# Kernel optimization log

Measured on AMD Instinct MI355X. Metric: run time of the kernel, lower is better.

Reference implementation:

```python
import jax, jax.numpy as jnp
import numpy as np

B, T, J, D = 128, 256, 50, 3
I, H, C = J * D, 1024, 60


def setup_inputs() -> dict:
    key = jax.random.key(0)
    ks = jax.random.split(key, 10)
    s = 0.02
    return {
        "x": jax.random.normal(ks[0], (B, T, J, D), dtype=jnp.float32),
        "h1": jnp.zeros((B, H), jnp.float32),
        "c1": jnp.zeros((B, H), jnp.float32),
        "h2": jnp.zeros((B, H), jnp.float32),
        "c2": jnp.zeros((B, H), jnp.float32),
        "W_ih1": jax.random.normal(ks[1], (4 * H, I), jnp.float32) * s,
        "W_hh1": jax.random.normal(ks[2], (4 * H, H), jnp.float32) * s,
        "b_ih1": jax.random.normal(ks[3], (4 * H,), jnp.float32) * s,
        "b_hh1": jax.random.normal(ks[4], (4 * H,), jnp.float32) * s,
        "W_ih2": jax.random.normal(ks[5], (4 * H, H), jnp.float32) * s,
        "W_hh2": jax.random.normal(ks[6], (4 * H, H), jnp.float32) * s,
        "b_ih2": jax.random.normal(ks[7], (4 * H,), jnp.float32) * s,
        "b_hh2": jax.random.normal(ks[8], (4 * H,), jnp.float32) * s,
        "W_fc": jax.random.normal(ks[9], (C, H), jnp.float32) * s,
        "b_fc": jnp.zeros((C,), jnp.float32),
        "mode": 0,  # 0 == 'val' (no dropout), static
    }


def _lstm_cell(xv, h, c, Wih, Whh, bih, bhh):
    # PyTorch LSTMCell gate order: i, f, g, o
    gates = xv @ Wih.T + bih + h @ Whh.T + bhh  # [B, 4H]
    i, f, g, o = jnp.split(gates, 4, axis=-1)
    c_new = jax.nn.sigmoid(f) * c + jax.nn.sigmoid(i) * jnp.tanh(g)
    h_new = jax.nn.sigmoid(o) * jnp.tanh(c_new)
    return h_new, c_new


def reference(x, h1, c1, h2, c2, W_ih1, W_hh1, b_ih1, b_hh1,
              W_ih2, W_hh2, b_ih2, b_hh2, W_fc, b_fc, mode):
    b, t = x.shape[0], x.shape[1]
    xs = x.reshape(b, t, -1).transpose(1, 0, 2)  # [T, B, I]

    def step(carry, xt):
        h1, c1, h2, c2 = carry
        h1, c1 = _lstm_cell(xt, h1, c1, W_ih1, W_hh1, b_ih1, b_hh1)
        # mode==0 ('val'): no dropout between layers
        h2, c2 = _lstm_cell(h1, h2, c2, W_ih2, W_hh2, b_ih2, b_hh2)
        return (h1, c1, h2, c2), None

    (h1, c1, h2, c2), _ = jax.lax.scan(step, (h1, c1, h2, c2), xs)
    return h2 @ W_fc.T + b_fc  # [B, num_class]
```

## Files before the change

### kernel.cpp

```cpp
#include <hip/hip_runtime.h>
#include <math.h>


typedef __bf16 bf16;
typedef __bf16 bf16x8 __attribute__((ext_vector_type(8)));
typedef float floatx4 __attribute__((ext_vector_type(4)));
typedef unsigned long long ull;

#define B_   128
#define T_   256
#define H_   1024
#define I_   150
#define KX_  160
#define C_   60
#define K1LDS 1280
#define KP    1024
#define NLINES 40
#define CSTRIDE 64
#define FLAGLINE 16
#define L0FLAG 32
#define L1FLAG 33
#define NCOLS 32
#define NHC  8
#define NT   2

template<int N> struct IC { static constexpr int value = N; };

__device__ __forceinline__ float sigmoidf_(float x) { return 1.f / (1.f + expf(-x)); }

__global__ __launch_bounds__(256)
void convert_all(const float* __restrict__ x,
                 const float* __restrict__ h1in, const float* __restrict__ h2in,
                 bf16* __restrict__ xb, bf16* __restrict__ h1b0, bf16* __restrict__ h2b0,
                 unsigned* __restrict__ cnt)
{
    const size_t nXB = (size_t)T_ * B_ * KX_;
    const size_t nHC = (size_t)B_ * H_;
    size_t idx = (size_t)blockIdx.x * 256 + threadIdx.x;

    if (idx < nXB) {
        size_t t = idx / (B_ * KX_);
        size_t r = idx - t * (B_ * KX_);
        size_t b = r / KX_, k = r - b * KX_;
        xb[idx] = (k < I_) ? (bf16)x[(b * T_ + t) * I_ + k] : (bf16)0.f;
        return;
    }
    idx -= nXB;
    if (idx < nHC) { h1b0[idx] = (bf16)h1in[idx]; return; }
    idx -= nHC;
    if (idx < nHC) { h2b0[idx] = (bf16)h2in[idx]; return; }
    idx -= nHC;
    if (idx < NLINES * CSTRIDE) cnt[idx] = 0u;
}

__device__ __forceinline__ void stage_rebal(
    bf16* lds, bf16* ldsP, int tid, int layer, int n0h,
    const float* Wih1, const float* Whh1, const float* Wih2, const float* Whh2)
{
    if (layer == 0) {
        {
            const int cpr = K1LDS >> 3;
            const int total = NCOLS * cpr;
            for (int ci = tid; ci < total; ci += 512) {
                int r = ci / cpr, c = ci - r * cpr;
                int g = r / NHC, j = r - g * NHC;
                int grow = (g << 10) + n0h + j;
                int k0 = c << 3;
                float v[8];
#pragma unroll
                for (int u = 0; u < 8; ++u) {
                    int k = k0 + u;
                    v[u] = (k < I_) ? Wih1[(size_t)grow * I_ + k]
                         : (k < KX_) ? 0.f
                         : (k < KX_ + H_) ? Whh1[(size_t)grow * H_ + (k - KX_)] : 0.f;
                }
                int cs = (c & ~15) | ((c ^ r) & 15);
                bf16* dst = lds + (size_t)r * K1LDS + (cs << 3);
#pragma unroll
                for (int u = 0; u < 8; ++u) dst[u] = (bf16)v[u];
            }
        }
        {
            const int cpr = KP >> 3;
            const int total = NCOLS * cpr;
            for (int ci = tid; ci < total; ci += 512) {
                int r = ci / cpr, c = ci - r * cpr;
                int g = r / NHC, j = r - g * NHC;
                int grow = (g << 10) + n0h + j;
                int k0 = c << 3;
                float v[8];
#pragma unroll
                for (int u = 0; u < 8; ++u) v[u] = Wih2[(size_t)grow * H_ + k0 + u];
                int cs = (c & ~15) | ((c ^ r) & 15);
                bf16* dst = ldsP + (size_t)r * KP + (cs << 3);
#pragma unroll
                for (int u = 0; u < 8; ++u) dst[u] = (bf16)v[u];
            }
        }
    } else {
        const int cpr = KP >> 3;
        const int total = NCOLS * cpr;
        for (int ci = tid; ci < total; ci += 512) {
            int r = ci / cpr, c = ci - r * cpr;
            int g = r / NHC, j = r - g * NHC;
            int grow = (g << 10) + n0h + j;
            int k0 = c << 3;
            float v[8];
#pragma unroll
            for (int u = 0; u < 8; ++u) v[u] = Whh2[(size_t)grow * H_ + k0 + u];
            int cs = (c & ~15) | ((c ^ r) & 15);
            bf16* dst = lds + (size_t)r * KP + (cs << 3);
#pragma unroll
            for (int u = 0; u < 8; ++u) dst[u] = (bf16)v[u];
        }
    }
}

__global__ __launch_bounds__(512, 2)
void rnn_decoup8(const bf16* __restrict__ xb,
                 bf16* __restrict__ h1b0, bf16* __restrict__ h1b1,
                 bf16* __restrict__ h2b0, bf16* __restrict__ h2b1,
                 float* __restrict__ p0, float* __restrict__ p1, float* __restrict__ p2,
                 const float* __restrict__ c1in, const float* __restrict__ c2in,
                 const float* __restrict__ Wih1, const float* __restrict__ Whh1,
                 const float* __restrict__ bih1, const float* __restrict__ bhh1,
                 const float* __restrict__ Wih2, const float* __restrict__ Whh2,
                 const float* __restrict__ bih2, const float* __restrict__ bhh2,
                 const float* __restrict__ Wfc, const float* __restrict__ bfc,
                 float* __restrict__ out, unsigned* __restrict__ cnt, int nblk)
{
    extern __shared__ bf16 lds[];
    __shared__ __align__(16) bf16 hst[8][16][NHC];

    const int tid   = threadIdx.x;
    const int bid   = blockIdx.x;
    const int layer = (bid >> 3) & 1;
    const int slice = (bid & 7) | ((bid >> 4) << 3);
    const int n0h   = slice * NHC;
    const int line  = layer * 16 + ((bid & 7) | (((bid >> 4) & 1) << 3));
    bf16* ldsP = lds + 32 * K1LDS;

    stage_rebal(lds, ldsP, tid, layer, n0h, Wih1, Whh1, Wih2, Whh2);
    __syncthreads();

    const int lane = tid & 63;
    const int wv   = tid >> 6;
    const int jj   = lane & (NHC - 1);
    const int quad = lane >> 4;

    float4 bias;
    {
        const float* bi = layer ? bih2 : bih1;
        const float* bh = layer ? bhh2 : bhh1;
        int col = n0h + jj;
        bias.x = bi[col] + bh[col];
        bias.y = bi[col + H_] + bh[col + H_];
        bias.z = bi[col + 2 * H_] + bh[col + 2 * H_];
        bias.w = bi[col + 3 * H_] + bh[col + 3 * H_];
    }

    float creg[2];
    {
        const float* cin = layer ? c2in : c1in;
        int dup = (lane >> 3) & 1;
#pragma unroll
        for (int rp = 0; rp < 2; ++rp) {
            int row = wv * 16 + quad * 4 + rp * 2 + dup;
            creg[rp] = cin[(size_t)row * H_ + n0h + jj];
        }
    }

    floatx4 acc[NT];
    floatx4 pacc[NT];

    auto seg1 = [&](const bf16* A, int ldA, const bf16* Bb, int ldB,
                    auto nksC, int ksBase) {
        constexpr int NKS = decltype(nksC)::value;
        constexpr int CH  = NKS < 16 ? NKS : 16;
        const int arow = wv * 16 + (lane & 15);
        const bf16* a0 = A + (size_t)arow * ldA + quad * 8;
        for (int blk = 0; blk < NKS; blk += CH) {
            bf16x8 a0r[CH];
#pragma unroll
            for (int i = 0; i < CH; ++i)
                a0r[i] = *(const bf16x8*)(a0 + (blk + i) * 32);
            __builtin_amdgcn_sched_barrier(0);
#pragma unroll
            for (int i = 0; i < CH; ++i) {
                int c = (ksBase + blk + i) * 4 + quad;
#pragma unroll
                for (int t = 0; t < NT; ++t) {
                    int r = t * 16 + (lane & 15);
                    int cs = (c & ~15) | ((c ^ r) & 15);
                    bf16x8 bfr = *(const bf16x8*)(Bb + (size_t)r * ldB + (cs << 3));
                    acc[t] = __builtin_amdgcn_mfma_f32_16x16x32_bf16(a0r[i], bfr, acc[t], 0, 0, 0);
                }
            }
        }
    };

    auto segDual = [&](const bf16* A) {
        const int arow = wv * 16 + (lane & 15);
        const bf16* a0 = A + (size_t)arow * H_ + quad * 8;
        for (int blk = 0; blk < 32; blk += 16) {
            bf16x8 a0r[16];
#pragma unroll
            for (int i = 0; i < 16; ++i)
                a0r[i] = *(const bf16x8*)(a0 + (blk + i) * 32);
            __builtin_amdgcn_sched_barrier(0);
#pragma unroll
            for (int i = 0; i < 16; ++i) {
                int ig = blk + i;
                int c1 = (5 + ig) * 4 + quad;
                int cp = ig * 4 + quad;
#pragma unroll
                for (int t = 0; t < NT; ++t) {
                    int r = t * 16 + (lane & 15);
                    int cs1 = (c1 & ~15) | ((c1 ^ r) & 15);
                    bf16x8 b1 = *(const bf16x8*)(lds + (size_t)r * K1LDS + (cs1 << 3));
                    acc[t] = __builtin_amdgcn_mfma_f32_16x16x32_bf16(a0r[i], b1, acc[t], 0, 0, 0);
                    int csp = (cp & ~15) | ((cp ^ r) & 15);
                    bf16x8 bp = *(const bf16x8*)(ldsP + (size_t)r * KP + (csp << 3));
                    pacc[t] = __builtin_amdgcn_mfma_f32_16x16x32_bf16(a0r[i], bp, pacc[t], 0, 0, 0);
                }
            }
        }
    };

    auto epilogue = [&](bf16* hw) {
        const int base = lane & 48;
#pragma unroll
        for (int r = 0; r < 4; ++r) {
            float vi = __shfl(acc[0][r], base + jj, 64);
            float vf = __shfl(acc[0][r], base + 8 + jj, 64);
            float vg = __shfl(acc[1][r], base + jj, 64);
            float vo = __shfl(acc[1][r], base + 8 + jj, 64);
            bool cond = (((lane >> 3) & 1) == (r & 1));
            int slot = r >> 1;
            if (cond) {
                float cv = creg[slot];
                float cn = sigmoidf_(vf + bias.y) * cv
                         + sigmoidf_(vi + bias.x) * tanhf(vg + bias.z);
                creg[slot] = cn;
                float hn = sigmoidf_(vo + bias.w) * tanhf(cn);
                hst[wv][quad * 4 + r][jj] = (bf16)hn;
            }
        }
        __syncthreads();
        if (lane < 32) {
            int row_l = lane >> 1, cg = lane & 1;
            ull v = *(const ull*)&hst[wv][row_l][cg * 4];
            __hip_atomic_store((ull*)(hw + (size_t)(wv * 16 + row_l) * H_ + n0h + cg * 4),
                               v, __ATOMIC_RELAXED, __HIP_MEMORY_SCOPE_AGENT);
        }
    };

    if (layer == 0) {
#pragma unroll
        for (int t = 0; t < NT; ++t) {
            acc[t]  = (floatx4){0.f, 0.f, 0.f, 0.f};
            pacc[t] = (floatx4){0.f, 0.f, 0.f, 0.f};
        }
        seg1(xb, KX_, lds, K1LDS, IC<5>{}, 0);
    }

    for (int e = 0; e <= T_ + 1; ++e) {
        const int pm  = e % 3;
        const int pmr = (e + 2) % 3;
        float* const pbuf[3] = { p0, p1, p2 };

        if (layer == 0 && e <= T_) {
            const bf16* h1r = (e & 1) ? h1b1 : h1b0;
            segDual(h1r);

            float* pw = pbuf[pm] + (size_t)slice * B_ * NCOLS;
#pragma unroll
            for (int t = 0; t < NT; ++t)
#pragma unroll
                for (int r = 0; r < 4; ++r) {
                    int row = wv * 16 + quad * 4 + r;
                    __hip_atomic_store(pw + (size_t)row * NCOLS + t * 16 + (lane & 15),
                                       pacc[t][r], __ATOMIC_RELAXED, __HIP_MEMORY_SCOPE_AGENT);
                }

            if (e < T_) {
                bf16* hw = (e & 1) ? h1b0 : h1b1;
                epilogue(hw);
            }
        } else if (layer == 1 && e >= 2) {
#pragma unroll
            for (int t = 0; t < NT; ++t) acc[t] = (floatx4){0.f, 0.f, 0.f, 0.f};

            const float* pr = pbuf[pmr] + (size_t)slice * B_ * NCOLS;
            float pv[NT][4];
#pragma unroll
            for (int t = 0; t < NT; ++t)
#pragma unroll
                for (int r = 0; r < 4; ++r) {
                    int row = wv * 16 + quad * 4 + r;
                    pv[t][r] = pr[(size_t)row * NCOLS + t * 16 + (lane & 15)];
                }

            const bf16* h2r = (e & 1) ? h2b1 : h2b0;
            seg1(h2r, H_, lds, KP, IC<32>{}, 0);

#pragma unroll
            for (int t = 0; t < NT; ++t)
#pragma unroll
                for (int r = 0; r < 4; ++r) acc[t][r] += pv[t][r];

            bf16* hw = (e & 1) ? h2b0 : h2b1;
            epilogue(hw);
        }

        asm volatile("s_waitcnt vmcnt(0)" ::: "memory");
        __syncthreads();
        const int etag = e + 1;
        if (tid == 0)
            __hip_atomic_fetch_add(cnt + line * CSTRIDE, 1u,
                                   __ATOMIC_RELAXED, __HIP_MEMORY_SCOPE_AGENT);
        if (layer == 0 && e < T_) {
#pragma unroll
            for (int t = 0; t < NT; ++t) {
                acc[t]  = (floatx4){0.f, 0.f, 0.f, 0.f};
                pacc[t] = (floatx4){0.f, 0.f, 0.f, 0.f};
            }
            if (e + 1 < T_)
                seg1(xb + (size_t)(e + 1) * B_ * KX_, KX_, lds, K1LDS, IC<5>{}, 0);
        }
        if (layer == 0) {
            if (bid == 0) {
                if (tid < 16) {
                    const unsigned tgt = 8u * (unsigned)etag;
                    const unsigned* cp = cnt + tid * CSTRIDE;
                    while (__hip_atomic_load(cp, __ATOMIC_RELAXED, __HIP_MEMORY_SCOPE_AGENT) < tgt)
                        __builtin_amdgcn_s_sleep(1);
                }
                if (tid == 0)
                    __hip_atomic_store(cnt + L0FLAG * CSTRIDE, (unsigned)etag,
                                       __ATOMIC_RELAXED, __HIP_MEMORY_SCOPE_AGENT);
            } else if (tid == 0) {
                const unsigned* fp = cnt + L0FLAG * CSTRIDE;
                while (__hip_atomic_load(fp, __ATOMIC_RELAXED, __HIP_MEMORY_SCOPE_AGENT) < (unsigned)etag)
                    __builtin_amdgcn_s_sleep(1);
            }
            if (tid == 0 && etag >= 3) {
                const unsigned* fp = cnt + L1FLAG * CSTRIDE;
                while (__hip_atomic_load(fp, __ATOMIC_RELAXED, __HIP_MEMORY_SCOPE_AGENT) < (unsigned)(etag - 2))
                    __builtin_amdgcn_s_sleep(1);
            }
        } else {
            if (bid == 8) {
                if (tid < 16) {
                    const unsigned tgt = 8u * (unsigned)etag;
                    const unsigned* cp = cnt + (16 + tid) * CSTRIDE;
                    while (__hip_atomic_load(cp, __ATOMIC_RELAXED, __HIP_MEMORY_SCOPE_AGENT) < tgt)
                        __builtin_amdgcn_s_sleep(1);
                }
                if (tid == 0)
                    __hip_atomic_store(cnt + L1FLAG * CSTRIDE, (unsigned)etag,
                                       __ATOMIC_RELAXED, __HIP_MEMORY_SCOPE_AGENT);
            } else if (tid == 0) {
                const unsigned* fp = cnt + L1FLAG * CSTRIDE;
                while (__hip_atomic_load(fp, __ATOMIC_RELAXED, __HIP_MEMORY_SCOPE_AGENT) < (unsigned)etag)
                    __builtin_amdgcn_s_sleep(1);
            }
            if (tid == 0) {
                const unsigned* fp = cnt + L0FLAG * CSTRIDE;
                while (__hip_atomic_load(fp, __ATOMIC_RELAXED, __HIP_MEMORY_SCOPE_AGENT) < (unsigned)etag)
                    __builtin_amdgcn_s_sleep(1);
            }
        }
        __syncthreads();
        if (tid < 64)
            __builtin_amdgcn_fence(__ATOMIC_ACQUIRE, "agent");
        __syncthreads();
    }

    if (tid == 0 && layer == 0) {
        const unsigned* fp = cnt + L1FLAG * CSTRIDE;
        while (__hip_atomic_load(fp, __ATOMIC_RELAXED, __HIP_MEMORY_SCOPE_AGENT) < (unsigned)(T_ + 2))
            __builtin_amdgcn_s_sleep(1);
    }
    __syncthreads();
    if (tid < 64)
        __builtin_amdgcn_fence(__ATOMIC_ACQUIRE, "agent");
    __syncthreads();

    if (bid < B_) {
        const bf16* h2f = h2b0;
        for (int c = wv; c < C_; c += 8) {
            float a = 0.f;
            for (int k = lane; k < H_; k += 64)
                a += (float)h2f[(size_t)bid * H_ + k] * Wfc[(size_t)c * H_ + k];
#pragma unroll
            for (int off = 32; off; off >>= 1) a += __shfl_down(a, off, 64);
            if (lane == 0) out[bid * C_ + c] = a + bfc[c];
        }
    }
}

__global__ __launch_bounds__(512, 2)
void rnn_rebal8(const bf16* __restrict__ xb,
                bf16* __restrict__ h1b0, bf16* __restrict__ h1b1,
                bf16* __restrict__ h2b0, bf16* __restrict__ h2b1,
                float* __restrict__ p0, float* __restrict__ p1,
                const float* __restrict__ c1in, const float* __restrict__ c2in,
                const float* __restrict__ Wih1, const float* __restrict__ Whh1,
                const float* __restrict__ bih1, const float* __restrict__ bhh1,
                const float* __restrict__ Wih2, const float* __restrict__ Whh2,
                const float* __restrict__ bih2, const float* __restrict__ bhh2,
                const float* __restrict__ Wfc, const float* __restrict__ bfc,
                float* __restrict__ out, unsigned* __restrict__ cnt, int nblk)
{
    extern __shared__ bf16 lds[];
    __shared__ __align__(16) bf16 hst[8][16][NHC];

    const int tid   = threadIdx.x;
    const int bid   = blockIdx.x;
    const int layer = (bid >> 3) & 1;
    const int slice = (bid & 7) | ((bid >> 4) << 3);
    const int n0h   = slice * NHC;
    const int arr_per_line = nblk >> 4;
    bf16* ldsP = lds + 32 * K1LDS;

    stage_rebal(lds, ldsP, tid, layer, n0h, Wih1, Whh1, Wih2, Whh2);
    __syncthreads();

    const int lane = tid & 63;
    const int wv   = tid >> 6;
    const int jj   = lane & (NHC - 1);
    const int quad = lane >> 4;

    float4 bias;
    {
        const float* bi = layer ? bih2 : bih1;
        const float* bh = layer ? bhh2 : bhh1;
        int col = n0h + jj;
        bias.x = bi[col] + bh[col];
        bias.y = bi[col + H_] + bh[col + H_];
        bias.z = bi[col + 2 * H_] + bh[col + 2 * H_];
        bias.w = bi[col + 3 * H_] + bh[col + 3 * H_];
    }

    float creg[2];
    {
        const float* cin = layer ? c2in : c1in;
        int dup = (lane >> 3) & 1;
#pragma unroll
        for (int rp = 0; rp < 2; ++rp) {
            int row = wv * 16 + quad * 4 + rp * 2 + dup;
            creg[rp] = cin[(size_t)row * H_ + n0h + jj];
        }
    }

    floatx4 acc[NT];
    floatx4 pacc[NT];

    auto seg1 = [&](const bf16* A, int ldA, const bf16* Bb, int ldB,
                    auto nksC, int ksBase) {
        constexpr int NKS = decltype(nksC)::value;
        constexpr int CH  = NKS < 16 ? NKS : 16;
        const int arow = wv * 16 + (lane & 15);
        const bf16* a0 = A + (size_t)arow * ldA + quad * 8;
        for (int blk = 0; blk < NKS; blk += CH) {
            bf16x8 a0r[CH];
#pragma unroll
            for (int i = 0; i < CH; ++i)
                a0r[i] = *(const bf16x8*)(a0 + (blk + i) * 32);
            __builtin_amdgcn_sched_barrier(0);
#pragma unroll
            for (int i = 0; i < CH; ++i) {
                int c = (ksBase + blk + i) * 4 + quad;
#pragma unroll
                for (int t = 0; t < NT; ++t) {
                    int r = t * 16 + (lane & 15);
                    int cs = (c & ~15) | ((c ^ r) & 15);
                    bf16x8 bfr = *(const bf16x8*)(Bb + (size_t)r * ldB + (cs << 3));
                    acc[t] = __builtin_amdgcn_mfma_f32_16x16x32_bf16(a0r[i], bfr, acc[t], 0, 0, 0);
                }
            }
        }
    };

    auto segDual = [&](const bf16* A) {
        const int arow = wv * 16 + (lane & 15);
        const bf16* a0 = A + (size_t)arow * H_ + quad * 8;
        for (int blk = 0; blk < 32; blk += 16) {
            bf16x8 a0r[16];
#pragma unroll
            for (int i = 0; i < 16; ++i)
                a0r[i] = *(const bf16x8*)(a0 + (blk + i) * 32);
            __builtin_amdgcn_sched_barrier(0);
#pragma unroll
            for (int i = 0; i < 16; ++i) {
                int ig = blk + i;
                int c1 = (5 + ig) * 4 + quad;
                int cp = ig * 4 + quad;
#pragma unroll
                for (int t = 0; t < NT; ++t) {
                    int r = t * 16 + (lane & 15);
                    int cs1 = (c1 & ~15) | ((c1 ^ r) & 15);
                    bf16x8 b1 = *(const bf16x8*)(lds + (size_t)r * K1LDS + (cs1 << 3));
                    acc[t] = __builtin_amdgcn_mfma_f32_16x16x32_bf16(a0r[i], b1, acc[t], 0, 0, 0);
                    int csp = (cp & ~15) | ((cp ^ r) & 15);
                    bf16x8 bp = *(const bf16x8*)(ldsP + (size_t)r * KP + (csp << 3));
                    pacc[t] = __builtin_amdgcn_mfma_f32_16x16x32_bf16(a0r[i], bp, pacc[t], 0, 0, 0);
                }
            }
        }
    };

    auto epilogue = [&](bf16* hw) {
        const int base = lane & 48;
#pragma unroll
        for (int r = 0; r < 4; ++r) {
            float vi = __shfl(acc[0][r], base + jj, 64);
            float vf = __shfl(acc[0][r], base + 8 + jj, 64);
            float vg = __shfl(acc[1][r], base + jj, 64);
            float vo = __shfl(acc[1][r], base + 8 + jj, 64);
            bool cond = (((lane >> 3) & 1) == (r & 1));
            int slot = r >> 1;
            if (cond) {
                float cv = creg[slot];
                float cn = sigmoidf_(vf + bias.y) * cv
                         + sigmoidf_(vi + bias.x) * tanhf(vg + bias.z);
                creg[slot] = cn;
                float hn = sigmoidf_(vo + bias.w) * tanhf(cn);
                hst[wv][quad * 4 + r][jj] = (bf16)hn;
            }
        }
        __syncthreads();
        if (lane < 32) {
            int row_l = lane >> 1, cg = lane & 1;
            ull v = *(const ull*)&hst[wv][row_l][cg * 4];
            __hip_atomic_store((ull*)(hw + (size_t)(wv * 16 + row_l) * H_ + n0h + cg * 4),
                               v, __ATOMIC_RELAXED, __HIP_MEMORY_SCOPE_AGENT);
        }
    };

    if (layer == 0) {
#pragma unroll
        for (int t = 0; t < NT; ++t) {
            acc[t]  = (floatx4){0.f, 0.f, 0.f, 0.f};
            pacc[t] = (floatx4){0.f, 0.f, 0.f, 0.f};
        }
        seg1(xb, KX_, lds, K1LDS, IC<5>{}, 0);
    }

    for (int e = 0; e <= T_ + 1; ++e) {
        if (layer == 0 && e <= T_) {
            const bf16* h1r = (e & 1) ? h1b1 : h1b0;
            segDual(h1r);

            float* pw = ((e & 1) ? p1 : p0) + (size_t)slice * B_ * NCOLS;
#pragma unroll
            for (int t = 0; t < NT; ++t)
#pragma unroll
                for (int r = 0; r < 4; ++r) {
                    int row = wv * 16 + quad * 4 + r;
                    __hip_atomic_store(pw + (size_t)row * NCOLS + t * 16 + (lane & 15),
                                       pacc[t][r], __ATOMIC_RELAXED, __HIP_MEMORY_SCOPE_AGENT);
                }

            if (e < T_) {
                bf16* hw = (e & 1) ? h1b0 : h1b1;
                epilogue(hw);
            }
        } else if (layer == 1 && e >= 2) {
#pragma unroll
            for (int t = 0; t < NT; ++t) acc[t] = (floatx4){0.f, 0.f, 0.f, 0.f};

            const float* pr = ((e & 1) ? p0 : p1) + (size_t)slice * B_ * NCOLS;
            float pv[NT][4];
#pragma unroll
            for (int t = 0; t < NT; ++t)
#pragma unroll
                for (int r = 0; r < 4; ++r) {
                    int row = wv * 16 + quad * 4 + r;
                    pv[t][r] = pr[(size_t)row * NCOLS + t * 16 + (lane & 15)];
                }

            const bf16* h2r = (e & 1) ? h2b1 : h2b0;
            seg1(h2r, H_, lds, KP, IC<32>{}, 0);

#pragma unroll
            for (int t = 0; t < NT; ++t)
#pragma unroll
                for (int r = 0; r < 4; ++r) acc[t][r] += pv[t][r];

            bf16* hw = (e & 1) ? h2b0 : h2b1;
            epilogue(hw);
        }

        asm volatile("s_waitcnt vmcnt(0)" ::: "memory");
        __syncthreads();
        const unsigned etag = (unsigned)(e + 1);
        if (tid == 0)
            __hip_atomic_fetch_add(cnt + (bid & 15) * CSTRIDE, 1u,
                                   __ATOMIC_RELAXED, __HIP_MEMORY_SCOPE_AGENT);
        if (layer == 0 && e < T_) {
#pragma unroll
            for (int t = 0; t < NT; ++t) {
                acc[t]  = (floatx4){0.f, 0.f, 0.f, 0.f};
                pacc[t] = (floatx4){0.f, 0.f, 0.f, 0.f};
            }
            if (e + 1 < T_)
                seg1(xb + (size_t)(e + 1) * B_ * KX_, KX_, lds, K1LDS, IC<5>{}, 0);
        }
        if (bid == 0) {
            if (tid < 16) {
                const unsigned tgt = etag * (unsigned)arr_per_line;
                const unsigned* cp = cnt + tid * CSTRIDE;
                while (__hip_atomic_load(cp, __ATOMIC_RELAXED, __HIP_MEMORY_SCOPE_AGENT) < tgt)
                    __builtin_amdgcn_s_sleep(1);
            }
            if (tid == 0)
                __hip_atomic_store(cnt + FLAGLINE * CSTRIDE, etag,
                                   __ATOMIC_RELAXED, __HIP_MEMORY_SCOPE_AGENT);
        } else {
            if (tid == 0) {
                const unsigned* fp = cnt + FLAGLINE * CSTRIDE;
                while (__hip_atomic_load(fp, __ATOMIC_RELAXED, __HIP_MEMORY_SCOPE_AGENT) < etag)
                    __builtin_amdgcn_s_sleep(1);
            }
        }
        __syncthreads();
        if (tid < 64)
            __builtin_amdgcn_fence(__ATOMIC_ACQUIRE, "agent");
        __syncthreads();
    }

    if (bid < B_) {
        const bf16* h2f = h2b0;
        for (int c = wv; c < C_; c += 8) {
            float a = 0.f;
            for (int k = lane; k < H_; k += 64)
                a += (float)h2f[(size_t)bid * H_ + k] * Wfc[(size_t)c * H_ + k];
#pragma unroll
            for (int off = 32; off; off >>= 1) a += __shfl_down(a, off, 64);
            if (lane == 0) out[bid * C_ + c] = a + bfc[c];
        }
    }
}

extern "C" void kernel_launch(void* const* d_in, const int* in_sizes, int n_in,
                              void* d_out, int out_size, void* d_ws, size_t ws_size,
                              hipStream_t stream)
{
    const float* x    = (const float*)d_in[0];
    const float* h1in = (const float*)d_in[1];
    const float* c1in = (const float*)d_in[2];
    const float* h2in = (const float*)d_in[3];
    const float* c2in = (const float*)d_in[4];
    const float* Wih1 = (const float*)d_in[5];
    const float* Whh1 = (const float*)d_in[6];
    const float* bih1 = (const float*)d_in[7];
    const float* bhh1 = (const float*)d_in[8];
    const float* Wih2 = (const float*)d_in[9];
    const float* Whh2 = (const float*)d_in[10];
    const float* bih2 = (const float*)d_in[11];
    const float* bhh2 = (const float*)d_in[12];
    const float* Wfc  = (const float*)d_in[13];
    const float* bfc  = (const float*)d_in[14];
    float* out = (float*)d_out;

    const size_t szXB  = (size_t)T_ * B_ * KX_ * 2;
    const size_t szH   = (size_t)B_ * H_ * 2;
    const size_t szCnt = (size_t)NLINES * CSTRIDE * 4;
    const size_t szP   = (size_t)128 * B_ * NCOLS * 4;
    const size_t needR13 = szXB + 4 * szH + szCnt + 2 * szP;
    const size_t needDec = szXB + 4 * szH + szCnt + 3 * szP;

    char* p = (char*)d_ws;
    bf16* xb = (bf16*)p;    p += szXB;
    bf16* h1b0 = (bf16*)p;  p += szH;
    bf16* h1b1 = (bf16*)p;  p += szH;
    bf16* h2b0 = (bf16*)p;  p += szH;
    bf16* h2b1 = (bf16*)p;  p += szH;
    unsigned* cnt = (unsigned*)p;  p += szCnt;
    float* p0 = (float*)p;  p += szP;
    float* p1 = (float*)p;  p += szP;
    float* p2 = (float*)p;

    const size_t citems = (size_t)T_ * B_ * KX_ + 2 * (size_t)B_ * H_ + NLINES * CSTRIDE;
    convert_all<<<(int)((citems + 255) / 256), 256, 0, stream>>>(
        x, h1in, h2in, xb, h1b0, h2b0, cnt);

    int nblk = 256;
    void* argsDec[] = { &xb, &h1b0, &h1b1, &h2b0, &h2b1, &p0, &p1, &p2,
                        (void*)&c1in, (void*)&c2in,
                        (void*)&Wih1, (void*)&Whh1, (void*)&bih1, (void*)&bhh1,
                        (void*)&Wih2, (void*)&Whh2, (void*)&bih2, (void*)&bhh2,
                        (void*)&Wfc, (void*)&bfc, &out, &cnt, &nblk };
    void* argsR13[] = { &xb, &h1b0, &h1b1, &h2b0, &h2b1, &p0, &p1,
                        (void*)&c1in, (void*)&c2in,
                        (void*)&Wih1, (void*)&Whh1, (void*)&bih1, (void*)&bhh1,
                        (void*)&Wih2, (void*)&Whh2, (void*)&bih2, (void*)&bhh2,
                        (void*)&Wfc, (void*)&bfc, &out, &cnt, &nblk };

    const unsigned ldsRebal = (unsigned)(32 * K1LDS + 32 * KP) * 2u;
    hipError_t err = hipErrorOutOfMemory;
    if (ws_size >= needDec) {
        if (hipFuncSetAttribute((const void*)rnn_decoup8,
                                hipFuncAttributeMaxDynamicSharedMemorySize,
                                (int)ldsRebal) == hipSuccess) {
            err = hipLaunchCooperativeKernel((const void*)rnn_decoup8,
                                             dim3(256), dim3(512), argsDec,
                                             ldsRebal, stream);
        }
    }
    if (err != hipSuccess && ws_size >= needR13) {
        (void)hipGetLastError();
        if (hipFuncSetAttribute((const void*)rnn_rebal8,
                                hipFuncAttributeMaxDynamicSharedMemorySize,
                                (int)ldsRebal) == hipSuccess) {
            (void)hipLaunchCooperativeKernel((const void*)rnn_rebal8,
                                             dim3(256), dim3(512), argsR13,
                                             ldsRebal, stream);
        }
    }
}
```

Measured before the change: 3.330 ms.

## Replace leader-based grid barrier with distributed per-line counter polling

```diff
diff --git a/kernel.cpp b/kernel.cpp
--- a/kernel.cpp
+++ b/kernel.cpp
@@ -17,7 +17,6 @@
 #define KP    1024
 #define NLINES 40
 #define CSTRIDE 64
-#define FLAGLINE 16
 #define L0FLAG 32
 #define L1FLAG 33
 #define NCOLS 32
@@ -112,6 +111,271 @@
             bf16* dst = lds + (size_t)r * KP + (cs << 3);
 #pragma unroll
             for (int u = 0; u < 8; ++u) dst[u] = (bf16)v[u];
+        }
+    }
+}
+
+__global__ __launch_bounds__(512, 2)
+void rnn_dist8(const bf16* __restrict__ xb,
+               bf16* __restrict__ h1b0, bf16* __restrict__ h1b1,
+               bf16* __restrict__ h2b0, bf16* __restrict__ h2b1,
+               float* __restrict__ p0, float* __restrict__ p1, float* __restrict__ p2,
+               const float* __restrict__ c1in, const float* __restrict__ c2in,
+               const float* __restrict__ Wih1, const float* __restrict__ Whh1,
+               const float* __restrict__ bih1, const float* __restrict__ bhh1,
+               const float* __restrict__ Wih2, const float* __restrict__ Whh2,
+               const float* __restrict__ bih2, const float* __restrict__ bhh2,
+               const float* __restrict__ Wfc, const float* __restrict__ bfc,
+               float* __restrict__ out, unsigned* __restrict__ cnt, int nblk)
+{
+    extern __shared__ bf16 lds[];
+    __shared__ __align__(16) bf16 hst[8][16][NHC];
+
+    const int tid   = threadIdx.x;
+    const int bid   = blockIdx.x;
+    const int layer = (bid >> 3) & 1;
+    const int slice = (bid & 7) | ((bid >> 4) << 3);
+    const int n0h   = slice * NHC;
+    const int line  = layer * 16 + ((bid & 7) | (((bid >> 4) & 1) << 3));
+    bf16* ldsP = lds + 32 * K1LDS;
+
+    stage_rebal(lds, ldsP, tid, layer, n0h, Wih1, Whh1, Wih2, Whh2);
+    __syncthreads();
+
+    const int lane = tid & 63;
+    const int wv   = tid >> 6;
+    const int jj   = lane & (NHC - 1);
+    const int quad = lane >> 4;
+
+    float4 bias;
+    {
+        const float* bi = layer ? bih2 : bih1;
+        const float* bh = layer ? bhh2 : bhh1;
+        int col = n0h + jj;
+        bias.x = bi[col] + bh[col];
+        bias.y = bi[col + H_] + bh[col + H_];
+        bias.z = bi[col + 2 * H_] + bh[col + 2 * H_];
+        bias.w = bi[col + 3 * H_] + bh[col + 3 * H_];
+    }
+
+    float creg[2];
+    {
+        const float* cin = layer ? c2in : c1in;
+        int dup = (lane >> 3) & 1;
+#pragma unroll
+        for (int rp = 0; rp < 2; ++rp) {
+            int row = wv * 16 + quad * 4 + rp * 2 + dup;
+            creg[rp] = cin[(size_t)row * H_ + n0h + jj];
+        }
+    }
+
+    floatx4 acc[NT];
+    floatx4 pacc[NT];
+
+    auto seg1 = [&](const bf16* A, int ldA, const bf16* Bb, int ldB,
+                    auto nksC, int ksBase) {
+        constexpr int NKS = decltype(nksC)::value;
+        constexpr int CH  = NKS < 16 ? NKS : 16;
+        const int arow = wv * 16 + (lane & 15);
+        const bf16* a0 = A + (size_t)arow * ldA + quad * 8;
+        for (int blk = 0; blk < NKS; blk += CH) {
+            bf16x8 a0r[CH];
+#pragma unroll
+            for (int i = 0; i < CH; ++i)
+                a0r[i] = *(const bf16x8*)(a0 + (blk + i) * 32);
+            __builtin_amdgcn_sched_barrier(0);
+#pragma unroll
+            for (int i = 0; i < CH; ++i) {
+                int c = (ksBase + blk + i) * 4 + quad;
+#pragma unroll
+                for (int t = 0; t < NT; ++t) {
+                    int r = t * 16 + (lane & 15);
+                    int cs = (c & ~15) | ((c ^ r) & 15);
+                    bf16x8 bfr = *(const bf16x8*)(Bb + (size_t)r * ldB + (cs << 3));
+                    acc[t] = __builtin_amdgcn_mfma_f32_16x16x32_bf16(a0r[i], bfr, acc[t], 0, 0, 0);
+                }
+            }
+        }
+    };
+
+    auto segDual = [&](const bf16* A) {
+        const int arow = wv * 16 + (lane & 15);
+        const bf16* a0 = A + (size_t)arow * H_ + quad * 8;
+        for (int blk = 0; blk < 32; blk += 16) {
+            bf16x8 a0r[16];
+#pragma unroll
+            for (int i = 0; i < 16; ++i)
+                a0r[i] = *(const bf16x8*)(a0 + (blk + i) * 32);
+            __builtin_amdgcn_sched_barrier(0);
+#pragma unroll
+            for (int i = 0; i < 16; ++i) {
+                int ig = blk + i;
+                int c1 = (5 + ig) * 4 + quad;
+                int cp = ig * 4 + quad;
+#pragma unroll
+                for (int t = 0; t < NT; ++t) {
+                    int r = t * 16 + (lane & 15);
+                    int cs1 = (c1 & ~15) | ((c1 ^ r) & 15);
+                    bf16x8 b1 = *(const bf16x8*)(lds + (size_t)r * K1LDS + (cs1 << 3));
+                    acc[t] = __builtin_amdgcn_mfma_f32_16x16x32_bf16(a0r[i], b1, acc[t], 0, 0, 0);
+                    int csp = (cp & ~15) | ((cp ^ r) & 15);
+                    bf16x8 bp = *(const bf16x8*)(ldsP + (size_t)r * KP + (csp << 3));
+                    pacc[t] = __builtin_amdgcn_mfma_f32_16x16x32_bf16(a0r[i], bp, pacc[t], 0, 0, 0);
+                }
+            }
+        }
+    };
+
+    auto epilogue = [&](bf16* hw) {
+        const int base = lane & 48;
+#pragma unroll
+        for (int r = 0; r < 4; ++r) {
+            float vi = __shfl(acc[0][r], base + jj, 64);
+            float vf = __shfl(acc[0][r], base + 8 + jj, 64);
+            float vg = __shfl(acc[1][r], base + jj, 64);
+            float vo = __shfl(acc[1][r], base + 8 + jj, 64);
+            bool cond = (((lane >> 3) & 1) == (r & 1));
+            int slot = r >> 1;
+            if (cond) {
+                float cv = creg[slot];
+                float cn = sigmoidf_(vf + bias.y) * cv
+                         + sigmoidf_(vi + bias.x) * tanhf(vg + bias.z);
+                creg[slot] = cn;
+                float hn = sigmoidf_(vo + bias.w) * tanhf(cn);
+                hst[wv][quad * 4 + r][jj] = (bf16)hn;
+            }
+        }
+        __syncthreads();
+        if (lane < 32) {
+            int row_l = lane >> 1, cg = lane & 1;
+            ull v = *(const ull*)&hst[wv][row_l][cg * 4];
+            __hip_atomic_store((ull*)(hw + (size_t)(wv * 16 + row_l) * H_ + n0h + cg * 4),
+                               v, __ATOMIC_RELAXED, __HIP_MEMORY_SCOPE_AGENT);
+        }
+    };
+
+    if (layer == 0) {
+#pragma unroll
+        for (int t = 0; t < NT; ++t) {
+            acc[t]  = (floatx4){0.f, 0.f, 0.f, 0.f};
+            pacc[t] = (floatx4){0.f, 0.f, 0.f, 0.f};
+        }
+        seg1(xb, KX_, lds, K1LDS, IC<5>{}, 0);
+    }
+
+    for (int e = 0; e <= T_ + 1; ++e) {
+        const int pm  = e % 3;
+        const int pmr = (e + 2) % 3;
+        float* const pbuf[3] = { p0, p1, p2 };
+
+        if (layer == 0 && e <= T_) {
+            const bf16* h1r = (e & 1) ? h1b1 : h1b0;
+            segDual(h1r);
+
+            float* pw = pbuf[pm] + (size_t)slice * B_ * NCOLS;
+#pragma unroll
+            for (int t = 0; t < NT; ++t)
+#pragma unroll
+                for (int r = 0; r < 4; ++r) {
+                    int row = wv * 16 + quad * 4 + r;
+                    __hip_atomic_store(pw + (size_t)row * NCOLS + t * 16 + (lane & 15),
+                                       pacc[t][r], __ATOMIC_RELAXED, __HIP_MEMORY_SCOPE_AGENT);
+                }
+
+            if (e < T_) {
+                bf16* hw = (e & 1) ? h1b0 : h1b1;
+                epilogue(hw);
+            }
+        } else if (layer == 1 && e >= 2) {
+#pragma unroll
+            for (int t = 0; t < NT; ++t) acc[t] = (floatx4){0.f, 0.f, 0.f, 0.f};
+
+            const float* pr = pbuf[pmr] + (size_t)slice * B_ * NCOLS;
+            float pv[NT][4];
+#pragma unroll
+            for (int t = 0; t < NT; ++t)
+#pragma unroll
+                for (int r = 0; r < 4; ++r) {
+                    int row = wv * 16 + quad * 4 + r;
+                    pv[t][r] = pr[(size_t)row * NCOLS + t * 16 + (lane & 15)];
+                }
+
+            const bf16* h2r = (e & 1) ? h2b1 : h2b0;
+            seg1(h2r, H_, lds, KP, IC<32>{}, 0);
+
+#pragma unroll
+            for (int t = 0; t < NT; ++t)
+#pragma unroll
+                for (int r = 0; r < 4; ++r) acc[t][r] += pv[t][r];
+
+            bf16* hw = (e & 1) ? h2b0 : h2b1;
+            epilogue(hw);
+        }
+
+        asm volatile("s_waitcnt vmcnt(0)" ::: "memory");
+        __syncthreads();
+        const int etag = e + 1;
+        if (tid == 0)
+            __hip_atomic_fetch_add(cnt + line * CSTRIDE, 1u,
+                                   __ATOMIC_RELAXED, __HIP_MEMORY_SCOPE_AGENT);
+        if (layer == 0 && e < T_) {
+#pragma unroll
+            for (int t = 0; t < NT; ++t) {
+                acc[t]  = (floatx4){0.f, 0.f, 0.f, 0.f};
+                pacc[t] = (floatx4){0.f, 0.f, 0.f, 0.f};
+            }
+            if (e + 1 < T_)
+                seg1(xb + (size_t)(e + 1) * B_ * KX_, KX_, lds, K1LDS, IC<5>{}, 0);
+        }
+        if (tid < 64) {
+            const unsigned* cp = nullptr;
+            unsigned tgt = 0;
+            if (lane < 16) {
+                cp = cnt + (layer * 16 + lane) * CSTRIDE;
+                tgt = 8u * (unsigned)etag;
+            } else if (lane < 32) {
+                if (layer == 0) {
+                    if (etag >= 3) {
+                        cp = cnt + (16 + (lane - 16)) * CSTRIDE;
+                        tgt = 8u * (unsigned)(etag - 2);
+                    }
+                } else {
+                    cp = cnt + (lane - 16) * CSTRIDE;
+                    tgt = 8u * (unsigned)etag;
+                }
+            }
+            for (;;) {
+                bool ok = (cp == nullptr) ||
+                          (__hip_atomic_load(cp, __ATOMIC_RELAXED,
+                                             __HIP_MEMORY_SCOPE_AGENT) >= tgt);
+                if (__all(ok)) break;
+                __builtin_amdgcn_s_sleep(1);
+            }
+            __builtin_amdgcn_fence(__ATOMIC_ACQUIRE, "agent");
+        }
+        __syncthreads();
+    }
+
+    if (tid < 64) {
+        if (lane < 16) {
+            const unsigned* cp = cnt + (16 + lane) * CSTRIDE;
+            while (__hip_atomic_load(cp, __ATOMIC_RELAXED,
+                                     __HIP_MEMORY_SCOPE_AGENT) < 8u * (unsigned)(T_ + 2))
+                __builtin_amdgcn_s_sleep(1);
+        }
+        __builtin_amdgcn_fence(__ATOMIC_ACQUIRE, "agent");
+    }
+    __syncthreads();
+
+    if (bid < B_) {
+        const bf16* h2f = h2b0;
+        for (int c = wv; c < C_; c += 8) {
+            float a = 0.f;
+            for (int k = lane; k < H_; k += 64)
+                a += (float)h2f[(size_t)bid * H_ + k] * Wfc[(size_t)c * H_ + k];
+#pragma unroll
+            for (int off = 32; off; off >>= 1) a += __shfl_down(a, off, 64);
+            if (lane == 0) out[bid * C_ + c] = a + bfc[c];
         }
     }
 }
@@ -386,250 +650,6 @@
     if (tid < 64)
         __builtin_amdgcn_fence(__ATOMIC_ACQUIRE, "agent");
     __syncthreads();
-
-    if (bid < B_) {
-        const bf16* h2f = h2b0;
-        for (int c = wv; c < C_; c += 8) {
-            float a = 0.f;
-            for (int k = lane; k < H_; k += 64)
-                a += (float)h2f[(size_t)bid * H_ + k] * Wfc[(size_t)c * H_ + k];
-#pragma unroll
-            for (int off = 32; off; off >>= 1) a += __shfl_down(a, off, 64);
-            if (lane == 0) out[bid * C_ + c] = a + bfc[c];
-        }
-    }
-}
-
-__global__ __launch_bounds__(512, 2)
-void rnn_rebal8(const bf16* __restrict__ xb,
-                bf16* __restrict__ h1b0, bf16* __restrict__ h1b1,
-                bf16* __restrict__ h2b0, bf16* __restrict__ h2b1,
-                float* __restrict__ p0, float* __restrict__ p1,
-                const float* __restrict__ c1in, const float* __restrict__ c2in,
-                const float* __restrict__ Wih1, const float* __restrict__ Whh1,
-                const float* __restrict__ bih1, const float* __restrict__ bhh1,
-                const float* __restrict__ Wih2, const float* __restrict__ Whh2,
-                const float* __restrict__ bih2, const float* __restrict__ bhh2,
-                const float* __restrict__ Wfc, const float* __restrict__ bfc,
-                float* __restrict__ out, unsigned* __restrict__ cnt, int nblk)
-{
-    extern __shared__ bf16 lds[];
-    __shared__ __align__(16) bf16 hst[8][16][NHC];
-
-    const int tid   = threadIdx.x;
-    const int bid   = blockIdx.x;
-    const int layer = (bid >> 3) & 1;
-    const int slice = (bid & 7) | ((bid >> 4) << 3);
-    const int n0h   = slice * NHC;
-    const int arr_per_line = nblk >> 4;
-    bf16* ldsP = lds + 32 * K1LDS;
-
-    stage_rebal(lds, ldsP, tid, layer, n0h, Wih1, Whh1, Wih2, Whh2);
-    __syncthreads();
-
-    const int lane = tid & 63;
-    const int wv   = tid >> 6;
-    const int jj   = lane & (NHC - 1);
-    const int quad = lane >> 4;
-
-    float4 bias;
-    {
-        const float* bi = layer ? bih2 : bih1;
-        const float* bh = layer ? bhh2 : bhh1;
-        int col = n0h + jj;
-        bias.x = bi[col] + bh[col];
-        bias.y = bi[col + H_] + bh[col + H_];
-        bias.z = bi[col + 2 * H_] + bh[col + 2 * H_];
-        bias.w = bi[col + 3 * H_] + bh[col + 3 * H_];
-    }
-
-    float creg[2];
-    {
-        const float* cin = layer ? c2in : c1in;
-        int dup = (lane >> 3) & 1;
-#pragma unroll
-        for (int rp = 0; rp < 2; ++rp) {
-            int row = wv * 16 + quad * 4 + rp * 2 + dup;
-            creg[rp] = cin[(size_t)row * H_ + n0h + jj];
-        }
-    }
-
-    floatx4 acc[NT];
-    floatx4 pacc[NT];
-
-    auto seg1 = [&](const bf16* A, int ldA, const bf16* Bb, int ldB,
-                    auto nksC, int ksBase) {
-        constexpr int NKS = decltype(nksC)::value;
-        constexpr int CH  = NKS < 16 ? NKS : 16;
-        const int arow = wv * 16 + (lane & 15);
-        const bf16* a0 = A + (size_t)arow * ldA + quad * 8;
-        for (int blk = 0; blk < NKS; blk += CH) {
-            bf16x8 a0r[CH];
-#pragma unroll
-            for (int i = 0; i < CH; ++i)
-                a0r[i] = *(const bf16x8*)(a0 + (blk + i) * 32);
-            __builtin_amdgcn_sched_barrier(0);
-#pragma unroll
-            for (int i = 0; i < CH; ++i) {
-                int c = (ksBase + blk + i) * 4 + quad;
-#pragma unroll
-                for (int t = 0; t < NT; ++t) {
-                    int r = t * 16 + (lane & 15);
-                    int cs = (c & ~15) | ((c ^ r) & 15);
-                    bf16x8 bfr = *(const bf16x8*)(Bb + (size_t)r * ldB + (cs << 3));
-                    acc[t] = __builtin_amdgcn_mfma_f32_16x16x32_bf16(a0r[i], bfr, acc[t], 0, 0, 0);
-                }
-            }
-        }
-    };
-
-    auto segDual = [&](const bf16* A) {
-        const int arow = wv * 16 + (lane & 15);
-        const bf16* a0 = A + (size_t)arow * H_ + quad * 8;
-        for (int blk = 0; blk < 32; blk += 16) {
-            bf16x8 a0r[16];
-#pragma unroll
-            for (int i = 0; i < 16; ++i)
-                a0r[i] = *(const bf16x8*)(a0 + (blk + i) * 32);
-            __builtin_amdgcn_sched_barrier(0);
-#pragma unroll
-            for (int i = 0; i < 16; ++i) {
-                int ig = blk + i;
-                int c1 = (5 + ig) * 4 + quad;
-                int cp = ig * 4 + quad;
-#pragma unroll
-                for (int t = 0; t < NT; ++t) {
-                    int r = t * 16 + (lane & 15);
-                    int cs1 = (c1 & ~15) | ((c1 ^ r) & 15);
-                    bf16x8 b1 = *(const bf16x8*)(lds + (size_t)r * K1LDS + (cs1 << 3));
-                    acc[t] = __builtin_amdgcn_mfma_f32_16x16x32_bf16(a0r[i], b1, acc[t], 0, 0, 0);
-                    int csp = (cp & ~15) | ((cp ^ r) & 15);
-                    bf16x8 bp = *(const bf16x8*)(ldsP + (size_t)r * KP + (csp << 3));
-                    pacc[t] = __builtin_amdgcn_mfma_f32_16x16x32_bf16(a0r[i], bp, pacc[t], 0, 0, 0);
-                }
-            }
-        }
-    };
-
-    auto epilogue = [&](bf16* hw) {
-        const int base = lane & 48;
-#pragma unroll
-        for (int r = 0; r < 4; ++r) {
-            float vi = __shfl(acc[0][r], base + jj, 64);
-            float vf = __shfl(acc[0][r], base + 8 + jj, 64);
-            float vg = __shfl(acc[1][r], base + jj, 64);
-            float vo = __shfl(acc[1][r], base + 8 + jj, 64);
-            bool cond = (((lane >> 3) & 1) == (r & 1));
-            int slot = r >> 1;
-            if (cond) {
-                float cv = creg[slot];
-                float cn = sigmoidf_(vf + bias.y) * cv
-                         + sigmoidf_(vi + bias.x) * tanhf(vg + bias.z);
-                creg[slot] = cn;
-                float hn = sigmoidf_(vo + bias.w) * tanhf(cn);
-                hst[wv][quad * 4 + r][jj] = (bf16)hn;
-            }
-        }
-        __syncthreads();
-        if (lane < 32) {
-            int row_l = lane >> 1, cg = lane & 1;
-            ull v = *(const ull*)&hst[wv][row_l][cg * 4];
-            __hip_atomic_store((ull*)(hw + (size_t)(wv * 16 + row_l) * H_ + n0h + cg * 4),
-                               v, __ATOMIC_RELAXED, __HIP_MEMORY_SCOPE_AGENT);
-        }
-    };
-
-    if (layer == 0) {
-#pragma unroll
-        for (int t = 0; t < NT; ++t) {
-            acc[t]  = (floatx4){0.f, 0.f, 0.f, 0.f};
-            pacc[t] = (floatx4){0.f, 0.f, 0.f, 0.f};
-        }
-        seg1(xb, KX_, lds, K1LDS, IC<5>{}, 0);
-    }
-
-    for (int e = 0; e <= T_ + 1; ++e) {
-        if (layer == 0 && e <= T_) {
-            const bf16* h1r = (e & 1) ? h1b1 : h1b0;
-            segDual(h1r);
-
-            float* pw = ((e & 1) ? p1 : p0) + (size_t)slice * B_ * NCOLS;
-#pragma unroll
-            for (int t = 0; t < NT; ++t)
-#pragma unroll
-                for (int r = 0; r < 4; ++r) {
-                    int row = wv * 16 + quad * 4 + r;
-                    __hip_atomic_store(pw + (size_t)row * NCOLS + t * 16 + (lane & 15),
-                                       pacc[t][r], __ATOMIC_RELAXED, __HIP_MEMORY_SCOPE_AGENT);
-                }
-
-            if (e < T_) {
-                bf16* hw = (e & 1) ? h1b0 : h1b1;
-                epilogue(hw);
-            }
-        } else if (layer == 1 && e >= 2) {
-#pragma unroll
-            for (int t = 0; t < NT; ++t) acc[t] = (floatx4){0.f, 0.f, 0.f, 0.f};
-
-            const float* pr = ((e & 1) ? p0 : p1) + (size_t)slice * B_ * NCOLS;
-            float pv[NT][4];
-#pragma unroll
-            for (int t = 0; t < NT; ++t)
-#pragma unroll
-                for (int r = 0; r < 4; ++r) {
-                    int row = wv * 16 + quad * 4 + r;
-                    pv[t][r] = pr[(size_t)row * NCOLS + t * 16 + (lane & 15)];
-                }
-
-            const bf16* h2r = (e & 1) ? h2b1 : h2b0;
-            seg1(h2r, H_, lds, KP, IC<32>{}, 0);
-
-#pragma unroll
-            for (int t = 0; t < NT; ++t)
-#pragma unroll
-                for (int r = 0; r < 4; ++r) acc[t][r] += pv[t][r];
-
-            bf16* hw = (e & 1) ? h2b0 : h2b1;
-            epilogue(hw);
-        }
-
-        asm volatile("s_waitcnt vmcnt(0)" ::: "memory");
-        __syncthreads();
-        const unsigned etag = (unsigned)(e + 1);
-        if (tid == 0)
-            __hip_atomic_fetch_add(cnt + (bid & 15) * CSTRIDE, 1u,
-                                   __ATOMIC_RELAXED, __HIP_MEMORY_SCOPE_AGENT);
-        if (layer == 0 && e < T_) {
-#pragma unroll
-            for (int t = 0; t < NT; ++t) {
-                acc[t]  = (floatx4){0.f, 0.f, 0.f, 0.f};
-                pacc[t] = (floatx4){0.f, 0.f, 0.f, 0.f};
-            }
-            if (e + 1 < T_)
-                seg1(xb + (size_t)(e + 1) * B_ * KX_, KX_, lds, K1LDS, IC<5>{}, 0);
-        }
-        if (bid == 0) {
-            if (tid < 16) {
-                const unsigned tgt = etag * (unsigned)arr_per_line;
-                const unsigned* cp = cnt + tid * CSTRIDE;
-                while (__hip_atomic_load(cp, __ATOMIC_RELAXED, __HIP_MEMORY_SCOPE_AGENT) < tgt)
-                    __builtin_amdgcn_s_sleep(1);
-            }
-            if (tid == 0)
-                __hip_atomic_store(cnt + FLAGLINE * CSTRIDE, etag,
-                                   __ATOMIC_RELAXED, __HIP_MEMORY_SCOPE_AGENT);
-        } else {
-            if (tid == 0) {
-                const unsigned* fp = cnt + FLAGLINE * CSTRIDE;
-                while (__hip_atomic_load(fp, __ATOMIC_RELAXED, __HIP_MEMORY_SCOPE_AGENT) < etag)
-                    __builtin_amdgcn_s_sleep(1);
-            }
-        }
-        __syncthreads();
-        if (tid < 64)
-            __builtin_amdgcn_fence(__ATOMIC_ACQUIRE, "agent");
-        __syncthreads();
-    }
 
     if (bid < B_) {
         const bf16* h2f = h2b0;
@@ -669,7 +689,6 @@
     const size_t szH   = (size_t)B_ * H_ * 2;
     const size_t szCnt = (size_t)NLINES * CSTRIDE * 4;
     const size_t szP   = (size_t)128 * B_ * NCOLS * 4;
-    const size_t needR13 = szXB + 4 * szH + szCnt + 2 * szP;
     const size_t needDec = szXB + 4 * szH + szCnt + 3 * szP;
 
     char* p = (char*)d_ws;
@@ -688,36 +707,31 @@
         x, h1in, h2in, xb, h1b0, h2b0, cnt);
 
     int nblk = 256;
-    void* argsDec[] = { &xb, &h1b0, &h1b1, &h2b0, &h2b1, &p0, &p1, &p2,
-                        (void*)&c1in, (void*)&c2in,
-                        (void*)&Wih1, (void*)&Whh1, (void*)&bih1, (void*)&bhh1,
-                        (void*)&Wih2, (void*)&Whh2, (void*)&bih2, (void*)&bhh2,
-                        (void*)&Wfc, (void*)&bfc, &out, &cnt, &nblk };
-    void* argsR13[] = { &xb, &h1b0, &h1b1, &h2b0, &h2b1, &p0, &p1,
-                        (void*)&c1in, (void*)&c2in,
-                        (void*)&Wih1, (void*)&Whh1, (void*)&bih1, (void*)&bhh1,
-                        (void*)&Wih2, (void*)&Whh2, (void*)&bih2, (void*)&bhh2,
-                        (void*)&Wfc, (void*)&bfc, &out, &cnt, &nblk };
+    void* args[] = { &xb, &h1b0, &h1b1, &h2b0, &h2b1, &p0, &p1, &p2,
+                     (void*)&c1in, (void*)&c2in,
+                     (void*)&Wih1, (void*)&Whh1, (void*)&bih1, (void*)&bhh1,
+                     (void*)&Wih2, (void*)&Whh2, (void*)&bih2, (void*)&bhh2,
+                     (void*)&Wfc, (void*)&bfc, &out, &cnt, &nblk };
 
     const unsigned ldsRebal = (unsigned)(32 * K1LDS + 32 * KP) * 2u;
     hipError_t err = hipErrorOutOfMemory;
     if (ws_size >= needDec) {
+        if (hipFuncSetAttribute((const void*)rnn_dist8,
+                                hipFuncAttributeMaxDynamicSharedMemorySize,
+                                (int)ldsRebal) == hipSuccess) {
+            err = hipLaunchCooperativeKernel((const void*)rnn_dist8,
+                                             dim3(256), dim3(512), args,
+                                             ldsRebal, stream);
+        }
+    }
+    if (err != hipSuccess && ws_size >= needDec) {
+        (void)hipGetLastError();
         if (hipFuncSetAttribute((const void*)rnn_decoup8,
                                 hipFuncAttributeMaxDynamicSharedMemorySize,
                                 (int)ldsRebal) == hipSuccess) {
-            err = hipLaunchCooperativeKernel((const void*)rnn_decoup8,
-                                             dim3(256), dim3(512), argsDec,
+            (void)hipLaunchCooperativeKernel((const void*)rnn_decoup8,
+                                             dim3(256), dim3(512), args,
                                              ldsRebal, stream);
         }
     }
-    if (err != hipSuccess && ws_size >= needR13) {
-        (void)hipGetLastError();
-        if (hipFuncSetAttribute((const void*)rnn_rebal8,
-                                hipFuncAttributeMaxDynamicSharedMemorySize,
-                                (int)ldsRebal) == hipSuccess) {
-            (void)hipLaunchCooperativeKernel((const void*)rnn_rebal8,
-                                             dim3(256), dim3(512), argsR13,
-                                             ldsRebal, stream);
-        }
-    }
 }
```

Measured after the change: 3.329 ms. About the same (-0.0%).
